# Performance work log

Measured on AMD Instinct MI355X. Metric: run time of the kernel, lower is better.

Reference implementation:

```python
import jax, jax.numpy as jnp
import numpy as np

DIM = 512
N = 1024          # num_patches == seq len
HEADS = 8
DIM_HEAD = 64
INNER = HEADS * DIM_HEAD
BATCH = 8


def setup_inputs() -> dict:
    key = jax.random.key(0)
    k1, k2, k3, k4, k5 = jax.random.split(key, 5)
    x = jax.random.normal(k1, (BATCH, N, DIM), dtype=jnp.float32)
    # nn.Linear(dim, inner*3, bias=False): store as [dim, 3*inner] for x @ W
    w_qkv = jax.random.normal(k2, (DIM, 3 * INNER), dtype=jnp.float32) * (DIM ** -0.5)
    # relative_bias_table: Parameter init'd to zeros in torch; use small randn so it matters
    bias_table = jax.random.normal(k3, (2 * N - 1, HEADS), dtype=jnp.float32) * 0.02
    w_out = jax.random.normal(k4, (INNER, DIM), dtype=jnp.float32) * (INNER ** -0.5)
    b_out = jax.random.normal(k5, (DIM,), dtype=jnp.float32) * 0.02
    return {"x": x, "w_qkv": w_qkv, "bias_table": bias_table, "w_out": w_out, "b_out": b_out}


def reference(x, w_qkv, bias_table, w_out, b_out):
    B, n, _ = x.shape
    scale = DIM_HEAD ** -0.5
    qkv = x @ w_qkv                                   # [B, n, 3*INNER]
    q, k, v = jnp.split(qkv, 3, axis=-1)
    def split_heads(t):
        return t.reshape(B, n, HEADS, DIM_HEAD).transpose(0, 2, 1, 3)  # [B, H, n, d]
    q, k, v = split_heads(q), split_heads(k), split_heads(v)
    dots = jnp.einsum('bhnd,bhmd->bhnm', q, k) * scale  # [B, H, n, n]
    # relative index: i - j + (n - 1)
    idx = jnp.arange(n)[:, None] - jnp.arange(n)[None, :] + (n - 1)  # [n, n]
    rel_bias = bias_table[idx]                        # [n, n, H]
    rel_bias = rel_bias.transpose(2, 0, 1)[None]      # [1, H, n, n]
    attn = jax.nn.softmax(dots + rel_bias, axis=-1)
    out = jnp.einsum('bhnm,bhmd->bhnd', attn, v)      # [B, H, n, d]
    out = out.transpose(0, 2, 1, 3).reshape(B, n, INNER)
    return out @ w_out + b_out
```

## Files before the change

kernel.cpp:

```cpp
#include <hip/hip_runtime.h>
#include <hip/hip_bf16.h>

typedef short bf16x8 __attribute__((ext_vector_type(8)));
typedef float floatx4 __attribute__((ext_vector_type(4)));
typedef float floatx16 __attribute__((ext_vector_type(16)));
typedef unsigned uintx4 __attribute__((ext_vector_type(4)));

typedef const __attribute__((address_space(1))) void gvoid_t;
typedef __attribute__((address_space(3))) void lvoid_t;

__device__ __forceinline__ void gload_lds16(const void* g, void* l) {
  __builtin_amdgcn_global_load_lds((gvoid_t*)g, (lvoid_t*)l, 16, 0, 0);
}

__device__ __forceinline__ unsigned short f2bf(float f) {
  union { float f; unsigned u; } c; c.f = f;
  unsigned u = c.u + 0x7FFFu + ((c.u >> 16) & 1u);
  return (unsigned short)(u >> 16);
}

#define LOG2E 1.44269504f

__global__ __launch_bounds__(256) void cast_f32_bf16(const float* __restrict__ in,
                                                     unsigned short* __restrict__ out, int n4) {
  int i = blockIdx.x * blockDim.x + threadIdx.x;
  if (i >= n4) return;
  float4 v = ((const float4*)in)[i];
  ushort4 o;
  o.x = f2bf(v.x); o.y = f2bf(v.y); o.z = f2bf(v.z); o.w = f2bf(v.w);
  ((ushort4*)out)[i] = o;
}

__global__ __launch_bounds__(256) void tcast_f32_bf16(const float* __restrict__ in,
                                                      unsigned short* __restrict__ out,
                                                      int K, int N) {
  int idx = blockIdx.x * blockDim.x + threadIdx.x;
  if (idx >= K * N) return;
  int k = idx / N, n = idx - k * N;
  out[n * K + k] = f2bf(in[idx]);
}

__global__ __launch_bounds__(256) void tbias_kernel(const float* __restrict__ btab,
                                                    float* __restrict__ btT) {
  int i = blockIdx.x * blockDim.x + threadIdx.x;
  if (i >= 2047 * 8) return;
  int idx = i >> 3, h = i & 7;
  btT[h * 2047 + idx] = btab[i] * LOG2E;
}

template <int EPI>
__global__ __launch_bounds__(256, 2) void gemm_bf16(
    const unsigned short* __restrict__ A,
    const unsigned short* __restrict__ Bt,
    int M, int N, int K,
    unsigned short* __restrict__ qo, unsigned short* __restrict__ ko,
    unsigned short* __restrict__ vo,
    float* __restrict__ out, const float* __restrict__ bias) {
  __shared__ alignas(16) unsigned short lA[128 * 64];
  __shared__ alignas(16) unsigned short lB[128 * 64];
  const int tid = threadIdx.x;
  const int wave = tid >> 6, lane = tid & 63;
  const int wr = wave >> 1, wc = wave & 1;
  const int lrow = lane & 15, lk = lane >> 4;
  const int m0 = blockIdx.x * 128, n0 = blockIdx.y * 128;

  floatx4 acc[4][4] = {};

  for (int k0 = 0; k0 < K; k0 += 64) {
    __syncthreads();
#pragma unroll
    for (int i = 0; i < 4; ++i) {
      int c = i * 256 + tid;
      int row = c >> 3, kc = c & 7;
      int ksw = (kc ^ (row & 7)) << 3;
      gload_lds16(A + (size_t)(m0 + row) * K + k0 + ksw,
                  &lA[(i * 256 + wave * 64) * 8]);
      gload_lds16(Bt + (size_t)(n0 + row) * K + k0 + ksw,
                  &lB[(i * 256 + wave * 64) * 8]);
    }
    __syncthreads();
#pragma unroll
    for (int f = 0; f < 2; ++f) {
      bf16x8 av[4], bv[4];
      int kc = lk + f * 4;
#pragma unroll
      for (int mt = 0; mt < 4; ++mt) {
        int r = wr * 64 + mt * 16 + lrow;
        av[mt] = *(const bf16x8*)&lA[r * 64 + ((kc ^ (r & 7)) << 3)];
      }
#pragma unroll
      for (int nt = 0; nt < 4; ++nt) {
        int r = wc * 64 + nt * 16 + lrow;
        bv[nt] = *(const bf16x8*)&lB[r * 64 + ((kc ^ (r & 7)) << 3)];
      }
#pragma unroll
      for (int mt = 0; mt < 4; ++mt)
#pragma unroll
        for (int nt = 0; nt < 4; ++nt)
          acc[mt][nt] = __builtin_amdgcn_mfma_f32_16x16x32_bf16(av[mt], bv[nt], acc[mt][nt], 0, 0, 0);
    }
  }

#pragma unroll
  for (int mt = 0; mt < 4; ++mt)
#pragma unroll
    for (int nt = 0; nt < 4; ++nt)
#pragma unroll
      for (int rg = 0; rg < 4; ++rg) {
        int m = m0 + wr * 64 + mt * 16 + lk * 4 + rg;
        int n = n0 + wc * 64 + nt * 16 + lrow;
        float v = acc[mt][nt][rg];
        if constexpr (EPI == 0) {
          int b = m >> 10, ii = m & 1023;
          int sect = n >> 9, r = n & 511;
          int h = r >> 6, d = r & 63;
          size_t bh = (size_t)((b << 3) + h);
          if (sect == 0)      qo[bh * 65536 + (size_t)ii * 64 + d] = f2bf(v * (0.125f * LOG2E));
          else if (sect == 1) ko[bh * 65536 + (size_t)ii * 64 + d] = f2bf(v);
          else                vo[bh * 65536 + (size_t)d * 1024 + ii] = f2bf(v);
        } else {
          out[(size_t)m * N + n] = v + bias[n];
        }
      }
}

__global__ __launch_bounds__(128, 2) void attn_kernel(
    const unsigned short* __restrict__ q,
    const unsigned short* __restrict__ kbuf,
    const unsigned short* __restrict__ vT,
    const float* __restrict__ btT,
    unsigned short* __restrict__ ao)
{
  __shared__ alignas(16) unsigned short lK[2][64 * 64];
  __shared__ float lbias[1088];
  const int tid = threadIdx.x, wave = tid >> 6, lane = tid & 63;
  const int il = lane & 31, hi = lane >> 5;
  const int lid = ((blockIdx.x & 7) << 7) | (blockIdx.x >> 3);
  const int bh = lid >> 4, qt = lid & 15;
  const int h = bh & 7, b = bh >> 3;
  const int qB = qt * 64;
  const int i_ = qB + wave * 32 + il;
  const size_t base = (size_t)bh * 65536;
  const unsigned short* vrow = vT + base;

  for (int t = tid; t < 1087; t += 128)
    lbias[t] = btT[h * 2047 + qB + t];

  bf16x8 qf[4];
#pragma unroll
  for (int kd = 0; kd < 4; ++kd)
    qf[kd] = *(const bf16x8*)(q + base + (size_t)i_ * 64 + kd * 16 + hi * 8);

#define STAGE_K(dst, jbase)                                                     \
  {                                                                             \
    _Pragma("unroll") for (int i = 0; i < 4; ++i) {                             \
      int c = i * 128 + tid;                                                    \
      int row = c >> 3, kc = c & 7;                                             \
      gload_lds16(kbuf + base + (size_t)((jbase) + row) * 64 + ((kc ^ (row & 7)) << 3), \
                  &(dst)[(i * 128 + wave * 64) * 8]);                           \
    }                                                                           \
  }

  STAGE_K(lK[0], 0);
  __syncthreads();

  floatx16 accA = {}, accB = {};
  float m_ = -1e30f, s_ = 0.f;
  const int bias_off = (i_ - qB) + 1023 - 4 * hi;
  int buf = 0;

  for (int t = 0; t < 16; ++t) {
    const int j0 = t * 64;
    if (t < 15) STAGE_K(lK[buf ^ 1], j0 + 64);

    bf16x8 vf0[4], vf1[4];
#pragma unroll
    for (int ks = 0; ks < 4; ++ks) {
      vf0[ks] = *(const bf16x8*)(vrow + (size_t)il * 1024 + j0 + ks * 16 + hi * 8);
      vf1[ks] = *(const bf16x8*)(vrow + (size_t)(32 + il) * 1024 + j0 + ks * 16 + hi * 8);
    }

    floatx16 st0 = {}, st1 = {};
#pragma unroll
    for (int kd = 0; kd < 4; ++kd) {
      const int kc = ((kd * 2 + hi) ^ (il & 7)) << 3;
      bf16x8 kf0 = *(const bf16x8*)&lK[buf][il * 64 + kc];
      bf16x8 kf1 = *(const bf16x8*)&lK[buf][(32 + il) * 64 + kc];
      st0 = __builtin_amdgcn_mfma_f32_32x32x16_bf16(kf0, qf[kd], st0, 0, 0, 0);
      st1 = __builtin_amdgcn_mfma_f32_32x32x16_bf16(kf1, qf[kd], st1, 0, 0, 0);
    }

    const int bb = bias_off - j0;
    float pm = -1e30f;
#pragma unroll
    for (int r = 0; r < 16; ++r) {
      const int jl = (r & 3) + 8 * (r >> 2);
      st0[r] += lbias[bb - jl];
      st1[r] += lbias[bb - 32 - jl];
      pm = fmaxf(pm, fmaxf(st0[r], st1[r]));
    }
    pm = fmaxf(pm, __shfl_xor(pm, 32, 64));
    if (!__all(pm - m_ <= 8.f)) {
      const float nm = fmaxf(m_, pm);
      const float fs = exp2f(m_ - nm);
      s_ *= fs; accA *= fs; accB *= fs;
      m_ = nm;
    }
    float rs = 0.f;
#pragma unroll
    for (int r = 0; r < 16; ++r) {
      st0[r] = exp2f(st0[r] - m_);
      st1[r] = exp2f(st1[r] - m_);
      rs += st0[r] + st1[r];
    }
    rs += __shfl_xor(rs, 32, 64);
    s_ += rs;

    unsigned pk[2][4][2];
#pragma unroll
    for (int g = 0; g < 4; ++g)
#pragma unroll
      for (int e2 = 0; e2 < 2; ++e2) {
        asm("v_cvt_pk_bf16_f32 %0, %1, %2"
            : "=v"(pk[0][g][e2]) : "v"(st0[4 * g + 2 * e2]), "v"(st0[4 * g + 2 * e2 + 1]));
        asm("v_cvt_pk_bf16_f32 %0, %1, %2"
            : "=v"(pk[1][g][e2]) : "v"(st1[4 * g + 2 * e2]), "v"(st1[4 * g + 2 * e2 + 1]));
      }
    bf16x8 pf[4];
#pragma unroll
    for (int ks = 0; ks < 4; ++ks) {
      const int jb = ks >> 1, gb = (ks & 1) * 2;
      uintx4 w;
#pragma unroll
      for (int e2 = 0; e2 < 2; ++e2) {
        unsigned v0 = pk[jb][gb][e2], v1 = pk[jb][gb + 1][e2];
        unsigned send = hi ? v0 : v1;
        unsigned recv = __shfl_xor(send, 32, 64);
        w[e2]     = hi ? recv : v0;
        w[2 + e2] = hi ? v1 : recv;
      }
      pf[ks] = *(bf16x8*)&w;
    }

#pragma unroll
    for (int ks = 0; ks < 4; ++ks) {
      accA = __builtin_amdgcn_mfma_f32_32x32x16_bf16(vf0[ks], pf[ks], accA, 0, 0, 0);
      accB = __builtin_amdgcn_mfma_f32_32x32x16_bf16(vf1[ks], pf[ks], accB, 0, 0, 0);
    }

    __syncthreads();
    buf ^= 1;
  }

  const float inv = 1.0f / s_;
  unsigned short* aor = ao + (size_t)(b * 1024 + i_) * 512 + h * 64 + 4 * hi;
#pragma unroll
  for (int rq = 0; rq < 4; ++rq) {
    uint2 u;
    asm("v_cvt_pk_bf16_f32 %0, %1, %2"
        : "=v"(u.x) : "v"(accA[4 * rq] * inv), "v"(accA[4 * rq + 1] * inv));
    asm("v_cvt_pk_bf16_f32 %0, %1, %2"
        : "=v"(u.y) : "v"(accA[4 * rq + 2] * inv), "v"(accA[4 * rq + 3] * inv));
    *(uint2*)(aor + 8 * rq) = u;
    asm("v_cvt_pk_bf16_f32 %0, %1, %2"
        : "=v"(u.x) : "v"(accB[4 * rq] * inv), "v"(accB[4 * rq + 1] * inv));
    asm("v_cvt_pk_bf16_f32 %0, %1, %2"
        : "=v"(u.y) : "v"(accB[4 * rq + 2] * inv), "v"(accB[4 * rq + 3] * inv));
    *(uint2*)(aor + 32 + 8 * rq) = u;
  }
}

extern "C" void kernel_launch(void* const* d_in, const int* in_sizes, int n_in,
                              void* d_out, int out_size, void* d_ws, size_t ws_size,
                              hipStream_t stream) {
  (void)in_sizes; (void)n_in; (void)out_size; (void)ws_size;
  const float* x      = (const float*)d_in[0];
  const float* w_qkv  = (const float*)d_in[1];
  const float* btab   = (const float*)d_in[2];
  const float* w_out  = (const float*)d_in[3];
  const float* b_out  = (const float*)d_in[4];
  float* out = (float*)d_out;

  char* ws = (char*)d_ws;
  unsigned short* xb    = (unsigned short*)(ws);
  unsigned short* wqkvT = (unsigned short*)(ws + 8388608);
  unsigned short* woutT = (unsigned short*)(ws + 9961472);
  unsigned short* qb    = (unsigned short*)(ws + 10485760);
  unsigned short* kb    = (unsigned short*)(ws + 18874368);
  unsigned short* vT    = (unsigned short*)(ws + 27262976);
  unsigned short* ao    = (unsigned short*)(ws + 35651584);
  float*          btT   = (float*)(ws + 44040192);

  hipLaunchKernelGGL(cast_f32_bf16, dim3(4096), dim3(256), 0, stream, x, xb, 1048576);
  hipLaunchKernelGGL(tcast_f32_bf16, dim3(3072), dim3(256), 0, stream, w_qkv, wqkvT, 512, 1536);
  hipLaunchKernelGGL(tcast_f32_bf16, dim3(1024), dim3(256), 0, stream, w_out, woutT, 512, 512);
  hipLaunchKernelGGL(tbias_kernel, dim3(64), dim3(256), 0, stream, btab, btT);

  hipLaunchKernelGGL((gemm_bf16<0>), dim3(64, 12), dim3(256), 0, stream,
                     xb, wqkvT, 8192, 1536, 512, qb, kb, vT, (float*)nullptr, (const float*)nullptr);

  hipLaunchKernelGGL(attn_kernel, dim3(1024), dim3(128), 0, stream, qb, kb, vT, btT, ao);

  hipLaunchKernelGGL((gemm_bf16<1>), dim3(64, 4), dim3(256), 0, stream,
                     ao, woutT, 8192, 512, 512,
                     (unsigned short*)nullptr, (unsigned short*)nullptr, (unsigned short*)nullptr,
                     out, b_out);
}
```

Measured before the change: 108.9 us.

## Split attention key range across two wave pairs and merge softmax partials

Each attention block now runs 4 waves: two wave pairs each process half of the key sequence (512 keys) with their own double-buffered K tiles. The pairs then merge their online-softmax states (max, sum, accumulators) through LDS before the bf16 output is written. This halves the serial loop length per wave and raises wave-level parallelism, at the cost of doubled LDS for K, an extra LDS reduction and barrier, and higher launch bounds that may constrain registers.

```diff
diff --git a/kernel.cpp b/kernel.cpp
--- a/kernel.cpp
+++ b/kernel.cpp
@@ -124,26 +124,28 @@
       }
 }
 
-__global__ __launch_bounds__(128, 2) void attn_kernel(
+__global__ __launch_bounds__(256, 4) void attn_kernel(
     const unsigned short* __restrict__ q,
     const unsigned short* __restrict__ kbuf,
     const unsigned short* __restrict__ vT,
     const float* __restrict__ btT,
     unsigned short* __restrict__ ao)
 {
-  __shared__ alignas(16) unsigned short lK[2][64 * 64];
+  __shared__ alignas(16) unsigned short lK[2][2][64 * 64];
   __shared__ float lbias[1088];
   const int tid = threadIdx.x, wave = tid >> 6, lane = tid & 63;
   const int il = lane & 31, hi = lane >> 5;
+  const int pr = wave >> 1;
+  const int wq = wave & 1;
   const int lid = ((blockIdx.x & 7) << 7) | (blockIdx.x >> 3);
   const int bh = lid >> 4, qt = lid & 15;
   const int h = bh & 7, b = bh >> 3;
   const int qB = qt * 64;
-  const int i_ = qB + wave * 32 + il;
+  const int i_ = qB + wq * 32 + il;
   const size_t base = (size_t)bh * 65536;
   const unsigned short* vrow = vT + base;
 
-  for (int t = tid; t < 1087; t += 128)
+  for (int t = tid; t < 1087; t += 256)
     lbias[t] = btT[h * 2047 + qB + t];
 
   bf16x8 qf[4];
@@ -154,14 +156,14 @@
 #define STAGE_K(dst, jbase)                                                     \
   {                                                                             \
     _Pragma("unroll") for (int i = 0; i < 4; ++i) {                             \
-      int c = i * 128 + tid;                                                    \
+      int c = i * 128 + wq * 64 + lane;                                         \
       int row = c >> 3, kc = c & 7;                                             \
       gload_lds16(kbuf + base + (size_t)((jbase) + row) * 64 + ((kc ^ (row & 7)) << 3), \
-                  &(dst)[(i * 128 + wave * 64) * 8]);                           \
+                  &(dst)[(i * 128 + wq * 64) * 8]);                             \
     }                                                                           \
   }
 
-  STAGE_K(lK[0], 0);
+  STAGE_K(lK[pr][0], pr * 512);
   __syncthreads();
 
   floatx16 accA = {}, accB = {};
@@ -169,9 +171,9 @@
   const int bias_off = (i_ - qB) + 1023 - 4 * hi;
   int buf = 0;
 
-  for (int t = 0; t < 16; ++t) {
-    const int j0 = t * 64;
-    if (t < 15) STAGE_K(lK[buf ^ 1], j0 + 64);
+  for (int t = 0; t < 8; ++t) {
+    const int j0 = pr * 512 + t * 64;
+    if (t < 7) STAGE_K(lK[pr][buf ^ 1], j0 + 64);
 
     bf16x8 vf0[4], vf1[4];
 #pragma unroll
@@ -184,8 +186,8 @@
 #pragma unroll
     for (int kd = 0; kd < 4; ++kd) {
       const int kc = ((kd * 2 + hi) ^ (il & 7)) << 3;
-      bf16x8 kf0 = *(const bf16x8*)&lK[buf][il * 64 + kc];
-      bf16x8 kf1 = *(const bf16x8*)&lK[buf][(32 + il) * 64 + kc];
+      bf16x8 kf0 = *(const bf16x8*)&lK[pr][buf][il * 64 + kc];
+      bf16x8 kf1 = *(const bf16x8*)&lK[pr][buf][(32 + il) * 64 + kc];
       st0 = __builtin_amdgcn_mfma_f32_32x32x16_bf16(kf0, qf[kd], st0, 0, 0, 0);
       st1 = __builtin_amdgcn_mfma_f32_32x32x16_bf16(kf1, qf[kd], st1, 0, 0, 0);
     }
@@ -252,21 +254,50 @@
     buf ^= 1;
   }
 
-  const float inv = 1.0f / s_;
-  unsigned short* aor = ao + (size_t)(b * 1024 + i_) * 512 + h * 64 + 4 * hi;
-#pragma unroll
-  for (int rq = 0; rq < 4; ++rq) {
-    uint2 u;
-    asm("v_cvt_pk_bf16_f32 %0, %1, %2"
-        : "=v"(u.x) : "v"(accA[4 * rq] * inv), "v"(accA[4 * rq + 1] * inv));
-    asm("v_cvt_pk_bf16_f32 %0, %1, %2"
-        : "=v"(u.y) : "v"(accA[4 * rq + 2] * inv), "v"(accA[4 * rq + 3] * inv));
-    *(uint2*)(aor + 8 * rq) = u;
-    asm("v_cvt_pk_bf16_f32 %0, %1, %2"
-        : "=v"(u.x) : "v"(accB[4 * rq] * inv), "v"(accB[4 * rq + 1] * inv));
-    asm("v_cvt_pk_bf16_f32 %0, %1, %2"
-        : "=v"(u.y) : "v"(accB[4 * rq + 2] * inv), "v"(accB[4 * rq + 3] * inv));
-    *(uint2*)(aor + 32 + 8 * rq) = u;
+  float* lu = (float*)&lK[0][0][0];
+  if (wave >= 2) {
+    float* slot = lu + (size_t)(wave - 2) * 2304 + lane * 36;
+#pragma unroll
+    for (int c = 0; c < 4; ++c) {
+      floatx4 t4a = { accA[4 * c], accA[4 * c + 1], accA[4 * c + 2], accA[4 * c + 3] };
+      floatx4 t4b = { accB[4 * c], accB[4 * c + 1], accB[4 * c + 2], accB[4 * c + 3] };
+      *(floatx4*)(slot + 4 * c) = t4a;
+      *(floatx4*)(slot + 16 + 4 * c) = t4b;
+    }
+    slot[32] = m_;
+    slot[33] = s_;
+  }
+  __syncthreads();
+  if (wave < 2) {
+    const float* slot = lu + (size_t)wave * 2304 + lane * 36;
+    floatx4 u2[8];
+#pragma unroll
+    for (int c = 0; c < 8; ++c) u2[c] = *(const floatx4*)(slot + 4 * c);
+    const float m2 = slot[32], s2 = slot[33];
+    const float mm = fmaxf(m_, m2);
+    const float a0 = exp2f(m_ - mm), a1 = exp2f(m2 - mm);
+    const float invs = 1.0f / (s_ * a0 + s2 * a1);
+    const float c0 = a0 * invs, c1 = a1 * invs;
+
+    unsigned short* aor = ao + (size_t)(b * 1024 + i_) * 512 + h * 64 + 4 * hi;
+#pragma unroll
+    for (int rq = 0; rq < 4; ++rq) {
+      float oa0 = accA[4 * rq] * c0 + u2[rq][0] * c1;
+      float oa1 = accA[4 * rq + 1] * c0 + u2[rq][1] * c1;
+      float oa2 = accA[4 * rq + 2] * c0 + u2[rq][2] * c1;
+      float oa3 = accA[4 * rq + 3] * c0 + u2[rq][3] * c1;
+      float ob0 = accB[4 * rq] * c0 + u2[4 + rq][0] * c1;
+      float ob1 = accB[4 * rq + 1] * c0 + u2[4 + rq][1] * c1;
+      float ob2 = accB[4 * rq + 2] * c0 + u2[4 + rq][2] * c1;
+      float ob3 = accB[4 * rq + 3] * c0 + u2[4 + rq][3] * c1;
+      uint2 u;
+      asm("v_cvt_pk_bf16_f32 %0, %1, %2" : "=v"(u.x) : "v"(oa0), "v"(oa1));
+      asm("v_cvt_pk_bf16_f32 %0, %1, %2" : "=v"(u.y) : "v"(oa2), "v"(oa3));
+      *(uint2*)(aor + 8 * rq) = u;
+      asm("v_cvt_pk_bf16_f32 %0, %1, %2" : "=v"(u.x) : "v"(ob0), "v"(ob1));
+      asm("v_cvt_pk_bf16_f32 %0, %1, %2" : "=v"(u.y) : "v"(ob2), "v"(ob3));
+      *(uint2*)(aor + 32 + 8 * rq) = u;
+    }
   }
 }
 
@@ -299,7 +330,7 @@
   hipLaunchKernelGGL((gemm_bf16<0>), dim3(64, 12), dim3(256), 0, stream,
                      xb, wqkvT, 8192, 1536, 512, qb, kb, vT, (float*)nullptr, (const float*)nullptr);
 
-  hipLaunchKernelGGL(attn_kernel, dim3(1024), dim3(128), 0, stream, qb, kb, vT, btT, ao);
+  hipLaunchKernelGGL(attn_kernel, dim3(1024), dim3(256), 0, stream, qb, kb, vT, btT, ao);
 
   hipLaunchKernelGGL((gemm_bf16<1>), dim3(64, 4), dim3(256), 0, stream,
                      ao, woutT, 8192, 512, 512,
```

New measurement: 128.8 us, median of 2. +18.3%, slower.
